# Optimization experiments

Hardware: AMD Instinct MI355X
Metric: run time of the kernel (lower is better)

The kernel has to match this reference:

```python
import jax, jax.numpy as jnp
import numpy as np

K = 3; STRIDE = 1; PAD = 1
IN_C = 256; OUT_C = 512
SPAN = K * K * IN_C        # 2304, im2col row count
M = 3                      # ALSH augmentation dims
TABLE_SIZE = 8             # hash buckets
R = 2.5                    # LSH bin width


def setup_inputs() -> dict:
    key = jax.random.key(0)
    k1, k2, k3, k4 = jax.random.split(key, 4)
    stdv = 1.0 / np.sqrt(SPAN)
    inp = jax.random.normal(k1, (16, IN_C, 56, 56), dtype=jnp.float32)
    kernels = jax.random.uniform(k2, (OUT_C, SPAN), minval=-stdv, maxval=stdv,
                                 dtype=jnp.float32)
    a_hash = jax.random.normal(k3, (SPAN + M,), dtype=jnp.float32)
    b_hash = jax.random.uniform(k4, (1,), dtype=jnp.float32) * R
    return {"input": inp, "kernels": kernels, "a_hash": a_hash,
            "b_hash": b_hash, "mode": 1}


def _P(x, m):
    # ALSH P-augmentation: append ||x||^(2^i), i=1..m, per row. x: [O, SPAN]
    n = jnp.linalg.norm(x, axis=1, keepdims=True)
    ext = jnp.concatenate([n ** (2 ** (i + 1)) for i in range(m)], axis=1)
    return jnp.concatenate([x, ext], axis=1)  # [O, SPAN+M]


def _bucket(vals, b, r, ts):
    # floor((v+b)/r) ; fmod ts ; abs  (matches torch fmod-then-abs semantics)
    idx = jnp.floor((vals + b) / r).astype(jnp.int32)
    return jnp.abs(jnp.fmod(idx, ts))


def _im2col_matr(x):
    # [N, C, H, W] -> [SPAN, N*H2*W2]
    n = x.shape[0]
    h2 = (x.shape[2] - K + 2 * PAD) // STRIDE + 1
    w2 = (x.shape[3] - K + 2 * PAD) // STRIDE + 1
    patches = jax.lax.conv_general_dilated_patches(
        x, (K, K), (STRIDE, STRIDE), [(PAD, PAD), (PAD, PAD)])  # [N, SPAN, H2, W2]
    return patches.reshape(n, SPAN, h2 * w2).transpose(1, 0, 2).reshape(SPAN, -1), h2, w2


def reference(input, kernels, a_hash, b_hash, mode):
    n = input.shape[0]
    patch_matr, h2, w2 = _im2col_matr(input)  # [SPAN, L]

    # ---- build ALSH table: bucket of each kernel row ----
    kvals = _P(kernels, M) @ a_hash           # [OUT_C]
    kbuck = _bucket(kvals, b_hash[0], R, TABLE_SIZE)

    # ---- vote: hash every unit-normalized patch column, take modal bucket ----
    unit = patch_matr / jnp.linalg.norm(patch_matr, axis=0, keepdims=True)
    q_ext = jnp.full((M, unit.shape[1]), 0.5, dtype=unit.dtype)
    votes = a_hash @ jnp.concatenate([unit, q_ext], axis=0)  # [L]
    vbuck = _bucket(votes, b_hash[0], R, TABLE_SIZE)
    counts = jnp.bincount(vbuck, length=TABLE_SIZE)
    bucket = int(jnp.argmax(counts))

    # ---- gather active kernel rows for that bucket (data-dependent) ----
    rows = np.sort(np.where(np.asarray(kbuck) == bucket)[0])
    if rows.size != 0:
        active = kernels[jnp.asarray(rows)]          # [oc, SPAN]
        out = active @ patch_matr                    # [oc, L]
        if mode:
            out = out / (float(rows.size) / OUT_C)
        oc = int(rows.size)
    else:
        out = kernels @ patch_matr
        oc = OUT_C

    out = out.reshape(oc, n, h2 * w2).transpose(1, 0, 2).reshape(n, oc, h2, w2)
    return (out, jnp.asarray(rows, dtype=jnp.int32))
```

## Files before the change

### kernel.cpp

```cpp
#include <hip/hip_runtime.h>
#include <math.h>

#define N_    16
#define C_    256
#define H_    56
#define W_    56
#define HW_   3136
#define NPIX  50176
#define OUTC  512
#define SPAN_ 2304
#define BLKPX 256
#define HSLOT 384

typedef unsigned short u16;
typedef unsigned int   u32;
typedef __attribute__((ext_vector_type(8))) short bf16x8;
typedef __attribute__((ext_vector_type(8))) unsigned short u16x8;
typedef __attribute__((ext_vector_type(4))) float f32x4;
typedef __attribute__((ext_vector_type(4))) unsigned short u16x4;

__device__ __forceinline__ u16 f2bf(float v) {
    u32 x = __float_as_uint(v);
    u32 r = (x + 0x7fffu + ((x >> 16) & 1u)) >> 16;
    return (u16)r;
}

__device__ __forceinline__ int bucketf(float v, float b) {
    int idx = (int)floorf((v + b) / 2.5f);
    int r = idx % 8;
    return r < 0 ? -r : r;
}

__global__ void kbucket_kernel(const float* __restrict__ kern,
                               const float* __restrict__ ah,
                               const float* __restrict__ bh,
                               int* __restrict__ kbuck) {
    int oc = blockIdx.x;
    const float* kr = kern + (size_t)oc * SPAN_;
    float dot = 0.f, ss = 0.f;
    for (int j = threadIdx.x; j < SPAN_; j += 64) {
        float kv = kr[j];
        dot += kv * ah[j];
        ss  += kv * kv;
    }
    for (int o = 32; o; o >>= 1) {
        dot += __shfl_down(dot, o);
        ss  += __shfl_down(ss, o);
    }
    if (threadIdx.x == 0) {
        float n2 = ss;
        float n4 = n2 * n2;
        float n8 = n4 * n4;
        float v = dot + n2 * ah[SPAN_] + n4 * ah[SPAN_ + 1] + n8 * ah[SPAN_ + 2];
        kbuck[oc] = bucketf(v, bh[0]);
    }
}

__global__ __launch_bounds__(256) void prep_fused(const float* __restrict__ x,
                                                  const float* __restrict__ ah,
                                                  u16* __restrict__ xp,
                                                  float* __restrict__ g,
                                                  float* __restrict__ s2) {
    __shared__ float aL[SPAN_];
    __shared__ u16 tl[64][68];
    __shared__ float red[4][64][10];
    int t = threadIdx.x;
    for (int j = t; j < SPAN_; j += 256) aL[j] = ah[j];

    int px0 = blockIdx.x * 64;
    int img = px0 / HW_;
    int hw0 = px0 - img * HW_;
    int px_l = t & 63;
    int cq   = t >> 6;
    float pg[9];
#pragma unroll
    for (int kk = 0; kk < 9; ++kk) pg[kk] = 0.f;
    float ps = 0.f;
    __syncthreads();

    for (int cb0 = 0; cb0 < 4; ++cb0) {
        int c0 = cb0 * 64;
#pragma unroll
        for (int rep = 0; rep < 16; ++rep) {
            int c_l = rep * 4 + cq;
            float v = x[((size_t)(img * C_ + c0 + c_l)) * HW_ + hw0 + px_l];
            tl[px_l][c_l] = f2bf(v);
            const float* ac = &aL[(c0 + c_l) * 9];
#pragma unroll
            for (int kk = 0; kk < 9; ++kk) pg[kk] += ac[kk] * v;
            ps += v * v;
        }
        __syncthreads();
        int c4  = t & 15;
        int pxs = t >> 4;
#pragma unroll
        for (int rep = 0; rep < 4; ++rep) {
            int pl = rep * 16 + pxs;
            u16x4 v4 = *(const u16x4*)(&tl[pl][c4 * 4]);
            *(u16x4*)(&xp[((size_t)(px0 + pl)) * C_ + c0 + c4 * 4]) = v4;
        }
        __syncthreads();
    }

#pragma unroll
    for (int kk = 0; kk < 9; ++kk) red[cq][px_l][kk] = pg[kk];
    red[cq][px_l][9] = ps;
    __syncthreads();
    for (int it = t; it < 640; it += 256) {
        int pl = it / 10;
        int j  = it - pl * 10;
        float s = red[0][pl][j] + red[1][pl][j] + red[2][pl][j] + red[3][pl][j];
        int q = px0 + pl;
        if (j < 9) g[(size_t)j * NPIX + q] = s;
        else       s2[q] = s;
    }
}

__global__ __launch_bounds__(256) void vote_kernel(const float* __restrict__ g,
                                                   const float* __restrict__ s2,
                                                   const float* __restrict__ ah,
                                                   const float* __restrict__ bh,
                                                   int* __restrict__ counts) {
    __shared__ int hist[8];
    if (threadIdx.x < 8) hist[threadIdx.x] = 0;
    __syncthreads();
    int q = blockIdx.x * 256 + threadIdx.x;
    int n = q / HW_;
    int p = q - n * HW_;
    int h = p / W_;
    int w = p - h * W_;
    float dot = 0.f, ss = 0.f;
#pragma unroll
    for (int kk = 0; kk < 9; ++kk) {
        int dh = kk / 3 - 1, dw = kk % 3 - 1;
        int hh = h + dh, ww = w + dw;
        if (hh >= 0 && hh < H_ && ww >= 0 && ww < W_) {
            int idx = n * HW_ + hh * W_ + ww;
            dot += g[(size_t)kk * NPIX + idx];
            ss  += s2[idx];
        }
    }
    float qext = 0.5f * (ah[SPAN_] + ah[SPAN_ + 1] + ah[SPAN_ + 2]);
    float v = dot / sqrtf(ss) + qext;
    int b = bucketf(v, bh[0]);
    atomicAdd(&hist[b], 1);
    __syncthreads();
    if (threadIdx.x < 8) atomicAdd(&counts[threadIdx.x], hist[threadIdx.x]);
}

__global__ __launch_bounds__(512) void select_kernel(const int* __restrict__ counts,
                                                     const int* __restrict__ kbuck,
                                                     int* __restrict__ rowsb,
                                                     int* __restrict__ meta,
                                                     float* __restrict__ out,
                                                     int oc_total) {
    __shared__ int sBest;
    __shared__ int sScan[512];
    int t = threadIdx.x;
    if (t == 0) {
        int best = 0, bc = counts[0];
        for (int i = 1; i < 8; ++i) {
            int c = counts[i];
            if (c > bc) { bc = c; best = i; }
        }
        sBest = best;
    }
    __syncthreads();
    int best = sBest;
    int flag = (kbuck[t] == best) ? 1 : 0;
    sScan[t] = flag;
    __syncthreads();
    for (int off = 1; off < 512; off <<= 1) {
        int add = (t >= off) ? sScan[t - off] : 0;
        __syncthreads();
        sScan[t] += add;
        __syncthreads();
    }
    int cnt = sScan[511];
    int pos = sScan[t] - flag;
    if (flag) rowsb[pos] = t;
    if (cnt == 0) rowsb[t] = t;
    else if (t >= cnt) rowsb[t] = 0;
    if (t == 0) {
        meta[0] = cnt;
        meta[1] = (cnt == 0) ? OUTC : cnt;
    }
    float* rout = out + (size_t)N_ * oc_total * HW_;
    int eff = (cnt == 0) ? OUTC : cnt;
    int nw = eff < oc_total ? eff : oc_total;
    if (cnt == 0) {
        if (t < nw) rout[t] = (float)t;
    } else if (flag && pos < nw) {
        rout[pos] = (float)t;
    }
}

__global__ __launch_bounds__(256) void prep_w(const float* __restrict__ kern,
                                              const int* __restrict__ rowsb,
                                              const int* __restrict__ meta,
                                              const int* __restrict__ mode,
                                              u16* __restrict__ wfrag, int nf4) {
    int e = blockIdx.x * 256 + threadIdx.x;
    int lane = e & 63;
    int t2 = e >> 6;
    int g = t2 % nf4;
    int s = t2 / nf4;
    int kk = s >> 3;
    int cb = s & 7;
    int q = lane >> 4;
    int mcol = lane & 15;
    int ocEff = meta[1];
    int cnt = meta[0];
    float scale = (mode[0] && cnt > 0) ? 512.0f / (float)cnt : 1.0f;
    int oc_i = g * 16 + mcol;
    bool valid = oc_i < ocEff;
    int row = valid ? rowsb[oc_i] : 0;
    const float* kr = kern + (size_t)row * SPAN_;
    u16 w8[8];
#pragma unroll
    for (int j = 0; j < 8; ++j) {
        int c = cb * 32 + q * 8 + j;
        float v = valid ? kr[c * 9 + kk] * scale : 0.f;
        w8[j] = f2bf(v);
    }
    u16* dst = wfrag + ((size_t)((s * nf4 + g) * 64 + lane)) * 8;
#pragma unroll
    for (int j = 0; j < 8; ++j) dst[j] = w8[j];
}

__global__ __launch_bounds__(256, 2) void conv_mfma(const u16* __restrict__ xp,
                                                    const u16* __restrict__ wfrag,
                                                    float* __restrict__ out,
                                                    int nf4, int oc_total, int nby) {
    __shared__ u16 halo[HSLOT * 32];

    int flat = blockIdx.x;
    int bx, by;
    int full = 192 * nby;
    if (flat < full) {
        int gsz = 8 * nby;
        int gi = flat / gsz;
        int tr = flat - gi * gsz;
        by = tr >> 3;
        bx = gi * 8 + (tr & 7);
    } else {
        int tr = flat - full;
        by = tr >> 2;
        bx = 192 + (tr & 3);
    }

    const int t = threadIdx.x;
    const int lane = t & 63;
    const int wv = t >> 6;
    const int pb = bx * BLKPX;
    const int fb = by * 4;
    const int lane15 = lane & 15;
    const int laneq  = lane >> 4;

    int hA[4], wA[4], aBase[4];
#pragma unroll
    for (int f = 0; f < 4; ++f) {
        int p = pb + wv * 64 + f * 16 + lane15;
        int img = p / HW_;
        int rp = p - img * HW_;
        hA[f] = rp / W_;
        wA[f] = rp - hA[f] * W_;
        aBase[f] = (wv * 64 + f * 16 + 57 + lane15) * 32 + laneq * 8;
    }

    f32x4 acc[4][4];
#pragma unroll
    for (int f = 0; f < 4; ++f)
#pragma unroll
        for (int gg = 0; gg < 4; ++gg) acc[f][gg] = (f32x4){0.f, 0.f, 0.f, 0.f};
    const bf16x8 zf = {0, 0, 0, 0, 0, 0, 0, 0};

    const int plb = t >> 2;
    const int cby = (t & 3) * 16;
    const char* xpb = (const char*)xp;

    u16x8 R[6], R2[6];
#pragma unroll
    for (int r = 0; r < 6; ++r) {
        int gpx = pb - 57 + r * 64 + plb;
        gpx = gpx < 0 ? 0 : (gpx >= NPIX ? NPIX - 1 : gpx);
        R[r] = *(const u16x8*)(xpb + (size_t)gpx * 512 + cby);
    }

    const size_t kkStride = (size_t)8 * nf4 * 512;

    for (int cb = 0; cb < 8; ++cb) {
        __syncthreads();
#pragma unroll
        for (int r = 0; r < 6; ++r)
            *(u16x8*)&halo[r * 2048 + t * 8] = R[r];
        __syncthreads();

        if (cb < 7) {
#pragma unroll
            for (int r = 0; r < 6; ++r) {
                int gpx = pb - 57 + r * 64 + plb;
                gpx = gpx < 0 ? 0 : (gpx >= NPIX ? NPIX - 1 : gpx);
                R2[r] = *(const u16x8*)(xpb + (size_t)gpx * 512 +
                                        (cb + 1) * 64 + cby);
            }
        }

        const u16* wcb = wfrag + ((size_t)cb * nf4 + fb) * 512 + lane * 8;
#pragma unroll
        for (int kk = 0; kk < 9; ++kk) {
            const int dh = kk / 3 - 1, dw = kk % 3 - 1;
            const int toff32 = (dh * W_ + dw) * 32;
            bf16x8 aX[4];
#pragma unroll
            for (int f = 0; f < 4; ++f) {
                int hh = hA[f] + dh, ww = wA[f] + dw;
                bool val = (hh >= 0) & (hh < H_) & (ww >= 0) & (ww < W_);
                bf16x8 a = *(const bf16x8*)&halo[aBase[f] + toff32];
                aX[f] = val ? a : zf;
            }
            const u16* wk = wcb + (size_t)kk * kkStride;
            bf16x8 bW[4];
#pragma unroll
            for (int gg = 0; gg < 4; ++gg)
                bW[gg] = *(const bf16x8*)(wk + (size_t)gg * 512);
#pragma unroll
            for (int gg = 0; gg < 4; ++gg)
#pragma unroll
                for (int f = 0; f < 4; ++f)
                    acc[f][gg] = __builtin_amdgcn_mfma_f32_16x16x32_bf16(
                        aX[f], bW[gg], acc[f][gg], 0, 0, 0);
        }
#pragma unroll
        for (int r = 0; r < 6; ++r) R[r] = R2[r];
    }

#pragma unroll
    for (int f = 0; f < 4; ++f) {
        int p0 = pb + wv * 64 + f * 16 + laneq * 4;
        int img0 = p0 / HW_;
        int hw0 = p0 - img0 * HW_;
#pragma unroll
        for (int gg = 0; gg < 4; ++gg) {
            int oc = (fb + gg) * 16 + lane15;
            if (oc < oc_total) {
                float* op = out + ((size_t)img0 * oc_total + oc) * HW_ + hw0;
                *(f32x4*)op = acc[f][gg];
            }
        }
    }
}

extern "C" void kernel_launch(void* const* d_in, const int* in_sizes, int n_in,
                              void* d_out, int out_size, void* d_ws, size_t ws_size,
                              hipStream_t stream) {
    const float* x    = (const float*)d_in[0];
    const float* kern = (const float*)d_in[1];
    const float* ah   = (const float*)d_in[2];
    const float* bh   = (const float*)d_in[3];
    const int*   mode = (const int*)d_in[4];
    float* out = (float*)d_out;

    int oc_total = (out_size % (N_ * HW_ + 1) == 0) ? out_size / (N_ * HW_ + 1)
                                                    : OUTC;
    int nfTot = (oc_total + 15) / 16;
    int nf4   = ((nfTot + 3) / 4) * 4;
    int nby   = nf4 / 4;

    u16*   xp     = (u16*)d_ws;
    u16*   wfrag  = xp + (size_t)NPIX * C_;
    float* g      = (float*)(wfrag + (size_t)72 * 32 * 64 * 8);
    float* s2     = g + (size_t)9 * NPIX;
    int*   counts = (int*)(s2 + NPIX);
    int*   kbuck  = counts + 8;
    int*   rowsb  = kbuck + OUTC;
    int*   meta   = rowsb + OUTC;

    hipMemsetAsync(counts, 0, 8 * sizeof(int), stream);

    prep_fused<<<NPIX / 64, 256, 0, stream>>>(x, ah, xp, g, s2);

    kbucket_kernel<<<OUTC, 64, 0, stream>>>(kern, ah, bh, kbuck);
    vote_kernel<<<NPIX / 256, 256, 0, stream>>>(g, s2, ah, bh, counts);
    select_kernel<<<1, 512, 0, stream>>>(counts, kbuck, rowsb, meta, out, oc_total);

    prep_w<<<18 * nf4, 256, 0, stream>>>(kern, rowsb, meta, mode, wfrag, nf4);

    conv_mfma<<<(NPIX / BLKPX) * nby, 256, 0, stream>>>(xp, wfrag, out, nf4,
                                                        oc_total, nby);
}
```

Before: 111.2 us.

## Shrink conv tiles to 128 threads with padded halo and fuse kbucket into vote

The MFMA conv kernel now runs 128-thread blocks over 128 pixels with four blocks per CU. Its halo buffer uses an 80-byte padded row stride, meant to cut LDS bank conflicts. Blocks are remapped with a simple interleaved swizzle, and the separate R2 prefetch registers are dropped in favour of reloading into R after the LDS store. The kernel-row bucket computation becomes 8 extra blocks of the vote kernel using float4 loads, which removes one launch. Smaller tiles raise occupancy and parallelism but cut per-block weight reuse and increase total weight-fragment traffic.

```diff
diff --git a/kernel.cpp b/kernel.cpp
--- a/kernel.cpp
+++ b/kernel.cpp
@@ -9,8 +9,9 @@
 #define NPIX  50176
 #define OUTC  512
 #define SPAN_ 2304
-#define BLKPX 256
-#define HSLOT 384
+#define BLKPX 128
+#define HSLOTS 256
+#define HSTRIDE 80
 
 typedef unsigned short u16;
 typedef unsigned int   u32;
@@ -29,31 +30,6 @@
     int idx = (int)floorf((v + b) / 2.5f);
     int r = idx % 8;
     return r < 0 ? -r : r;
-}
-
-__global__ void kbucket_kernel(const float* __restrict__ kern,
-                               const float* __restrict__ ah,
-                               const float* __restrict__ bh,
-                               int* __restrict__ kbuck) {
-    int oc = blockIdx.x;
-    const float* kr = kern + (size_t)oc * SPAN_;
-    float dot = 0.f, ss = 0.f;
-    for (int j = threadIdx.x; j < SPAN_; j += 64) {
-        float kv = kr[j];
-        dot += kv * ah[j];
-        ss  += kv * kv;
-    }
-    for (int o = 32; o; o >>= 1) {
-        dot += __shfl_down(dot, o);
-        ss  += __shfl_down(ss, o);
-    }
-    if (threadIdx.x == 0) {
-        float n2 = ss;
-        float n4 = n2 * n2;
-        float n8 = n4 * n4;
-        float v = dot + n2 * ah[SPAN_] + n4 * ah[SPAN_ + 1] + n8 * ah[SPAN_ + 2];
-        kbuck[oc] = bucketf(v, bh[0]);
-    }
 }
 
 __global__ __launch_bounds__(256) void prep_fused(const float* __restrict__ x,
@@ -116,11 +92,40 @@
     }
 }
 
-__global__ __launch_bounds__(256) void vote_kernel(const float* __restrict__ g,
-                                                   const float* __restrict__ s2,
-                                                   const float* __restrict__ ah,
-                                                   const float* __restrict__ bh,
-                                                   int* __restrict__ counts) {
+__global__ __launch_bounds__(256) void votek_kernel(const float* __restrict__ g,
+                                                    const float* __restrict__ s2,
+                                                    const float* __restrict__ ah,
+                                                    const float* __restrict__ bh,
+                                                    const float* __restrict__ kern,
+                                                    int* __restrict__ counts,
+                                                    int* __restrict__ kbuck) {
+    int kb = blockIdx.x - (NPIX / 256);
+    if (kb >= 0) {
+        int t = threadIdx.x;
+        int oc_l = t >> 2, part = t & 3;
+        int oc = kb * 64 + oc_l;
+        const float* kr = kern + (size_t)oc * SPAN_ + part * 576;
+        const float* ap = ah + part * 576;
+        float dot = 0.f, ss = 0.f;
+        for (int i = 0; i < 144; ++i) {
+            float4 kv = *(const float4*)(kr + i * 4);
+            float4 av = *(const float4*)(ap + i * 4);
+            dot += kv.x * av.x + kv.y * av.y + kv.z * av.z + kv.w * av.w;
+            ss  += kv.x * kv.x + kv.y * kv.y + kv.z * kv.z + kv.w * kv.w;
+        }
+        dot += __shfl_xor(dot, 1); dot += __shfl_xor(dot, 2);
+        ss  += __shfl_xor(ss, 1);  ss  += __shfl_xor(ss, 2);
+        if (part == 0) {
+            float n2 = ss;
+            float n4 = n2 * n2;
+            float n8 = n4 * n4;
+            float v = dot + n2 * ah[SPAN_] + n4 * ah[SPAN_ + 1] +
+                      n8 * ah[SPAN_ + 2];
+            kbuck[oc] = bucketf(v, bh[0]);
+        }
+        return;
+    }
+
     __shared__ int hist[8];
     if (threadIdx.x < 8) hist[threadIdx.x] = 0;
     __syncthreads();
@@ -228,26 +233,18 @@
     for (int j = 0; j < 8; ++j) dst[j] = w8[j];
 }
 
-__global__ __launch_bounds__(256, 2) void conv_mfma(const u16* __restrict__ xp,
+__global__ __launch_bounds__(128, 4) void conv_mfma(const u16* __restrict__ xp,
                                                     const u16* __restrict__ wfrag,
                                                     float* __restrict__ out,
                                                     int nf4, int oc_total, int nby) {
-    __shared__ u16 halo[HSLOT * 32];
-
-    int flat = blockIdx.x;
-    int bx, by;
-    int full = 192 * nby;
-    if (flat < full) {
-        int gsz = 8 * nby;
-        int gi = flat / gsz;
-        int tr = flat - gi * gsz;
-        by = tr >> 3;
-        bx = gi * 8 + (tr & 7);
-    } else {
-        int tr = flat - full;
-        by = tr >> 2;
-        bx = 192 + (tr & 3);
-    }
+    __shared__ char halo[HSLOTS * HSTRIDE];
+
+    const int tot = (NPIX / BLKPX) * nby;
+    const int q8 = tot >> 3;
+    const int flat = blockIdx.x;
+    const int virt = (flat & 7) * q8 + (flat >> 3);
+    const int bx = virt / nby;
+    const int by = virt - bx * nby;
 
     const int t = threadIdx.x;
     const int lane = t & 63;
@@ -265,7 +262,7 @@
         int rp = p - img * HW_;
         hA[f] = rp / W_;
         wA[f] = rp - hA[f] * W_;
-        aBase[f] = (wv * 64 + f * 16 + 57 + lane15) * 32 + laneq * 8;
+        aBase[f] = (57 + wv * 64 + f * 16 + lane15) * HSTRIDE + laneq * 16;
     }
 
     f32x4 acc[4][4];
@@ -275,48 +272,48 @@
         for (int gg = 0; gg < 4; ++gg) acc[f][gg] = (f32x4){0.f, 0.f, 0.f, 0.f};
     const bf16x8 zf = {0, 0, 0, 0, 0, 0, 0, 0};
 
-    const int plb = t >> 2;
-    const int cby = (t & 3) * 16;
+    const int splb = t >> 2;
+    const int sq   = (t & 3) * 16;
     const char* xpb = (const char*)xp;
-
-    u16x8 R[6], R2[6];
-#pragma unroll
-    for (int r = 0; r < 6; ++r) {
-        int gpx = pb - 57 + r * 64 + plb;
-        gpx = gpx < 0 ? 0 : (gpx >= NPIX ? NPIX - 1 : gpx);
-        R[r] = *(const u16x8*)(xpb + (size_t)gpx * 512 + cby);
-    }
+    int gpx[8];
+#pragma unroll
+    for (int r = 0; r < 8; ++r) {
+        int p = pb - 57 + r * 32 + splb;
+        gpx[r] = p < 0 ? 0 : (p >= NPIX ? NPIX - 1 : p);
+    }
+
+    u16x8 R[8];
+#pragma unroll
+    for (int r = 0; r < 8; ++r)
+        R[r] = *(const u16x8*)(xpb + (size_t)gpx[r] * 512 + sq);
 
     const size_t kkStride = (size_t)8 * nf4 * 512;
 
     for (int cb = 0; cb < 8; ++cb) {
         __syncthreads();
 #pragma unroll
-        for (int r = 0; r < 6; ++r)
-            *(u16x8*)&halo[r * 2048 + t * 8] = R[r];
+        for (int r = 0; r < 8; ++r)
+            *(u16x8*)&halo[(r * 32 + splb) * HSTRIDE + sq] = R[r];
         __syncthreads();
 
         if (cb < 7) {
 #pragma unroll
-            for (int r = 0; r < 6; ++r) {
-                int gpx = pb - 57 + r * 64 + plb;
-                gpx = gpx < 0 ? 0 : (gpx >= NPIX ? NPIX - 1 : gpx);
-                R2[r] = *(const u16x8*)(xpb + (size_t)gpx * 512 +
-                                        (cb + 1) * 64 + cby);
-            }
+            for (int r = 0; r < 8; ++r)
+                R[r] = *(const u16x8*)(xpb + (size_t)gpx[r] * 512 +
+                                       (cb + 1) * 64 + sq);
         }
 
         const u16* wcb = wfrag + ((size_t)cb * nf4 + fb) * 512 + lane * 8;
 #pragma unroll
         for (int kk = 0; kk < 9; ++kk) {
             const int dh = kk / 3 - 1, dw = kk % 3 - 1;
-            const int toff32 = (dh * W_ + dw) * 32;
+            const int toff = (dh * W_ + dw) * HSTRIDE;
             bf16x8 aX[4];
 #pragma unroll
             for (int f = 0; f < 4; ++f) {
                 int hh = hA[f] + dh, ww = wA[f] + dw;
                 bool val = (hh >= 0) & (hh < H_) & (ww >= 0) & (ww < W_);
-                bf16x8 a = *(const bf16x8*)&halo[aBase[f] + toff32];
+                bf16x8 a = *(const bf16x8*)&halo[aBase[f] + toff];
                 aX[f] = val ? a : zf;
             }
             const u16* wk = wcb + (size_t)kk * kkStride;
@@ -331,8 +328,6 @@
                     acc[f][gg] = __builtin_amdgcn_mfma_f32_16x16x32_bf16(
                         aX[f], bW[gg], acc[f][gg], 0, 0, 0);
         }
-#pragma unroll
-        for (int r = 0; r < 6; ++r) R[r] = R2[r];
     }
 
 #pragma unroll
@@ -380,12 +375,12 @@
 
     prep_fused<<<NPIX / 64, 256, 0, stream>>>(x, ah, xp, g, s2);
 
-    kbucket_kernel<<<OUTC, 64, 0, stream>>>(kern, ah, bh, kbuck);
-    vote_kernel<<<NPIX / 256, 256, 0, stream>>>(g, s2, ah, bh, counts);
+    votek_kernel<<<NPIX / 256 + 8, 256, 0, stream>>>(g, s2, ah, bh, kern,
+                                                     counts, kbuck);
     select_kernel<<<1, 512, 0, stream>>>(counts, kbuck, rowsb, meta, out, oc_total);
 
     prep_w<<<18 * nf4, 256, 0, stream>>>(kern, rowsb, meta, mode, wfrag, nf4);
 
-    conv_mfma<<<(NPIX / BLKPX) * nby, 256, 0, stream>>>(xp, wfrag, out, nf4,
+    conv_mfma<<<(NPIX / BLKPX) * nby, 128, 0, stream>>>(xp, wfrag, out, nf4,
                                                         oc_total, nby);
 }
```

New measurement: 167.6 us. 1.51x slower.

## Double-buffer halo via async global-to-LDS loads and prefetch weight fragments

Applied to the files above, without the earlier changes.

Replaces the register-staged halo copy with direct global_load_lds transfers into a double-buffered LDS halo. This removes one barrier and the register-to-LDS store per channel block. It also prefetches the next kernel-tap weight fragments one kk step ahead to hide global load latency behind the MFMAs. The cost is doubled LDS use, which may reduce occupancy, and correctness relies on the async LDS writes being complete before the next barrier.

```diff
diff --git a/kernel.cpp b/kernel.cpp
--- a/kernel.cpp
+++ b/kernel.cpp
@@ -10,7 +10,7 @@
 #define OUTC  512
 #define SPAN_ 2304
 #define BLKPX 256
-#define HSLOT 384
+#define HBYTES 24576
 
 typedef unsigned short u16;
 typedef unsigned int   u32;
@@ -232,7 +232,7 @@
                                                     const u16* __restrict__ wfrag,
                                                     float* __restrict__ out,
                                                     int nf4, int oc_total, int nby) {
-    __shared__ u16 halo[HSLOT * 32];
+    __shared__ char halo[2 * HBYTES];
 
     int flat = blockIdx.x;
     int bx, by;
@@ -265,7 +265,7 @@
         int rp = p - img * HW_;
         hA[f] = rp / W_;
         wA[f] = rp - hA[f] * W_;
-        aBase[f] = (wv * 64 + f * 16 + 57 + lane15) * 32 + laneq * 8;
+        aBase[f] = (57 + wv * 64 + f * 16 + lane15) * 64 + laneq * 16;
     }
 
     f32x4 acc[4][4];
@@ -275,64 +275,76 @@
         for (int gg = 0; gg < 4; ++gg) acc[f][gg] = (f32x4){0.f, 0.f, 0.f, 0.f};
     const bf16x8 zf = {0, 0, 0, 0, 0, 0, 0, 0};
 
-    const int plb = t >> 2;
-    const int cby = (t & 3) * 16;
     const char* xpb = (const char*)xp;
-
-    u16x8 R[6], R2[6];
+    const char* gsrc[6];
 #pragma unroll
     for (int r = 0; r < 6; ++r) {
-        int gpx = pb - 57 + r * 64 + plb;
-        gpx = gpx < 0 ? 0 : (gpx >= NPIX ? NPIX - 1 : gpx);
-        R[r] = *(const u16x8*)(xpb + (size_t)gpx * 512 + cby);
-    }
+        int p = pb - 57 + r * 64 + (t >> 2);
+        p = p < 0 ? 0 : (p >= NPIX ? NPIX - 1 : p);
+        gsrc[r] = xpb + (size_t)p * 512 + (t & 3) * 16;
+    }
+
+#pragma unroll
+    for (int r = 0; r < 6; ++r)
+        __builtin_amdgcn_global_load_lds(
+            (const __attribute__((address_space(1))) unsigned int*)(gsrc[r]),
+            (__attribute__((address_space(3))) unsigned int*)&halo[r * 4096 + t * 16],
+            16, 0, 0);
 
     const size_t kkStride = (size_t)8 * nf4 * 512;
 
     for (int cb = 0; cb < 8; ++cb) {
         __syncthreads();
-#pragma unroll
-        for (int r = 0; r < 6; ++r)
-            *(u16x8*)&halo[r * 2048 + t * 8] = R[r];
-        __syncthreads();
+        const char* hb = &halo[(cb & 1) * HBYTES];
 
         if (cb < 7) {
-#pragma unroll
-            for (int r = 0; r < 6; ++r) {
-                int gpx = pb - 57 + r * 64 + plb;
-                gpx = gpx < 0 ? 0 : (gpx >= NPIX ? NPIX - 1 : gpx);
-                R2[r] = *(const u16x8*)(xpb + (size_t)gpx * 512 +
-                                        (cb + 1) * 64 + cby);
+            char* hn = &halo[((cb + 1) & 1) * HBYTES];
+#pragma unroll
+            for (int r = 0; r < 6; ++r)
+                __builtin_amdgcn_global_load_lds(
+                    (const __attribute__((address_space(1))) unsigned int*)
+                        (gsrc[r] + (cb + 1) * 64),
+                    (__attribute__((address_space(3))) unsigned int*)
+                        &hn[r * 4096 + t * 16],
+                    16, 0, 0);
+        }
+
+        const u16* wcb = wfrag + ((size_t)cb * nf4 + fb) * 512 + lane * 8;
+        bf16x8 bW[4];
+#pragma unroll
+        for (int gg = 0; gg < 4; ++gg)
+            bW[gg] = *(const bf16x8*)(wcb + (size_t)gg * 512);
+
+#pragma unroll
+        for (int kk = 0; kk < 9; ++kk) {
+            bf16x8 bWn[4];
+            if (kk < 8) {
+                const u16* wn = wcb + (size_t)(kk + 1) * kkStride;
+#pragma unroll
+                for (int gg = 0; gg < 4; ++gg)
+                    bWn[gg] = *(const bf16x8*)(wn + (size_t)gg * 512);
             }
-        }
-
-        const u16* wcb = wfrag + ((size_t)cb * nf4 + fb) * 512 + lane * 8;
-#pragma unroll
-        for (int kk = 0; kk < 9; ++kk) {
             const int dh = kk / 3 - 1, dw = kk % 3 - 1;
-            const int toff32 = (dh * W_ + dw) * 32;
+            const int toff = (dh * W_ + dw) * 64;
             bf16x8 aX[4];
 #pragma unroll
             for (int f = 0; f < 4; ++f) {
                 int hh = hA[f] + dh, ww = wA[f] + dw;
                 bool val = (hh >= 0) & (hh < H_) & (ww >= 0) & (ww < W_);
-                bf16x8 a = *(const bf16x8*)&halo[aBase[f] + toff32];
+                bf16x8 a = *(const bf16x8*)&hb[aBase[f] + toff];
                 aX[f] = val ? a : zf;
             }
-            const u16* wk = wcb + (size_t)kk * kkStride;
-            bf16x8 bW[4];
-#pragma unroll
-            for (int gg = 0; gg < 4; ++gg)
-                bW[gg] = *(const bf16x8*)(wk + (size_t)gg * 512);
 #pragma unroll
             for (int gg = 0; gg < 4; ++gg)
 #pragma unroll
                 for (int f = 0; f < 4; ++f)
                     acc[f][gg] = __builtin_amdgcn_mfma_f32_16x16x32_bf16(
                         aX[f], bW[gg], acc[f][gg], 0, 0, 0);
-        }
-#pragma unroll
-        for (int r = 0; r < 6; ++r) R[r] = R2[r];
+            if (kk < 8) {
+#pragma unroll
+                for (int gg = 0; gg < 4; ++gg) bW[gg] = bWn[gg];
+            }
+        }
     }
 
 #pragma unroll
```

Measured after the change: 109.5 us. About the same (-1.5%).
